# Kernel optimization log

Hardware: AMD Instinct MI355X
Metric: run time of the kernel (lower is better)

Reference implementation:

```python
import jax, jax.numpy as jnp
import numpy as np

N_HEADS = 16
HEAD_DIM = 64
ROPE_BASE = 10000.0
EPS = 1e-6


def _rope_tables(T, hd, dtype):
    inv_freq = 1.0 / (ROPE_BASE ** (jnp.arange(0, hd, 2, dtype=jnp.float32) / hd))
    freqs = jnp.arange(T, dtype=jnp.float32)[:, None] * inv_freq[None, :]  # [T, hd/2]
    cos = jnp.cos(freqs)[None, :, None, :].astype(dtype)  # [1,T,1,hd/2]
    sin = jnp.sin(freqs)[None, :, None, :].astype(dtype)
    return cos, sin


def _apply_rope(x, cos, sin):
    d = x.shape[-1] // 2
    x1, x2 = x[..., :d], x[..., d:]
    return jnp.concatenate([x1 * cos + x2 * sin, -x1 * sin + x2 * cos], axis=-1)


def setup_inputs() -> dict:
    key = jax.random.key(0)
    k1, k2, k3, k4 = jax.random.split(key, 4)
    B, T, C = 4, 1024, 1024
    x = jax.random.normal(k1, (B, T, C), dtype=jnp.float32)
    W_qkv = jax.random.normal(k2, (3 * C, C), dtype=jnp.float32) * (1.0 / np.sqrt(C))
    W_out = jax.random.normal(k3, (C, C), dtype=jnp.float32) * (1.0 / np.sqrt(C))
    # learnable per-head curvature, init = exp(randn) * base_curvature (base=1.0)
    hyp_k = jnp.exp(jax.random.normal(k4, (1, N_HEADS, 1, 1), dtype=jnp.float32))
    return {"x": x, "W_qkv": W_qkv, "W_out": W_out, "hyp_k": hyp_k}


def reference(x, W_qkv, W_out, hyp_k):
    B, T, C = x.shape
    H, hd = N_HEADS, HEAD_DIM
    qkv = x @ W_qkv.T  # [B,T,3C]
    q, k, v = jnp.split(qkv, 3, axis=-1)
    q = q.reshape(B, T, H, hd)
    k = k.reshape(B, T, H, hd)
    v = v.reshape(B, T, H, hd)

    cos, sin = _rope_tables(T, hd, x.dtype)
    q = _apply_rope(q, cos, sin)
    k = _apply_rope(k, cos, sin)

    # [B,H,T,hd]
    q = q.transpose(0, 2, 1, 3)
    k = k.transpose(0, 2, 1, 3)
    v = v.transpose(0, 2, 1, 3)

    # Lorentz lift: x0 = sqrt(k + ||x||^2); inner = -x0*y0 + <x,y>;
    # dist = sqrt(k) * arccosh(-inner / k)  (geoopt Lorentz convention)
    kc = hyp_k[:, :, :, 0]  # [1,H,1]
    q0 = jnp.sqrt(kc + jnp.sum(q * q, axis=-1))  # [B,H,T]
    k0 = jnp.sqrt(kc + jnp.sum(k * k, axis=-1))  # [B,H,T]
    inner = jnp.einsum('bhld,bhsd->bhls', q, k) - q0[..., None] * k0[:, :, None, :]
    arg = jnp.maximum(-inner / hyp_k, 1.0 + EPS)
    dis = jnp.sqrt(hyp_k) * jnp.arccosh(arg)  # [B,H,L,S]

    attn_weight = 1.0 / (EPS + dis)
    causal = jnp.tril(jnp.ones((T, T), dtype=bool))
    attn_weight = jnp.where(causal, attn_weight, -jnp.inf)
    attn = jax.nn.softmax(attn_weight, axis=-1)
    out = jnp.einsum('bhls,bhsd->bhld', attn, v)  # [B,H,T,hd]
    out = out.transpose(0, 2, 1, 3).reshape(B, T, C)
    return out @ W_out.T
```

## Files before the change

kernel.cpp:

```cpp
#include <hip/hip_runtime.h>

#define B_ 4
#define T_ 1024
#define C_ 1024
#define H_ 16
#define HD_ 64

typedef short bf16x8 __attribute__((ext_vector_type(8)));
typedef float f32x4 __attribute__((ext_vector_type(4)));

__device__ __forceinline__ ushort f2bf(float f) {
    union { float f; unsigned u; } v; v.f = f;
    unsigned u = v.u;
    unsigned r = (u + 0x7fffu + ((u >> 16) & 1u)) >> 16;
    return (ushort)r;
}

__device__ __forceinline__ f32x4 mfma16(bf16x8 a, bf16x8 b, f32x4 c) {
    return __builtin_amdgcn_mfma_f32_16x16x32_bf16(a, b, c, 0, 0, 0);
}

__device__ __forceinline__ bf16x8 lds_frag(const ushort* base, int row, int byteoff) {
    int addr = (row * 128 + byteoff) ^ ((row & 7) << 4);
    uint4 u = *(const uint4*)((const char*)base + addr);
    return __builtin_bit_cast(bf16x8, u);
}

__device__ __forceinline__ bf16x8 lds_frag_v(const ushort* base, int d, int byteoff) {
    int addr = (d * 128 + byteoff) ^ ((((d & 7) ^ (d >> 3)) & 7) << 4);
    uint4 u = *(const uint4*)((const char*)base + addr);
    return __builtin_bit_cast(bf16x8, u);
}

__device__ __forceinline__ bf16x8 lds_frag_p(const ushort* base, int row, int byteoff) {
    int addr = (row * 128 + byteoff) ^ (((row >> 2) & 3) << 5);
    uint4 u = *(const uint4*)((const char*)base + addr);
    return __builtin_bit_cast(bf16x8, u);
}

__device__ __forceinline__ void bar_plain() {
    __builtin_amdgcn_sched_barrier(0);
    __builtin_amdgcn_s_barrier();
    __builtin_amdgcn_sched_barrier(0);
}
__device__ __forceinline__ void bar_vm6() {
    asm volatile("s_waitcnt vmcnt(6)" ::: "memory");
    __builtin_amdgcn_sched_barrier(0);
    __builtin_amdgcn_s_barrier();
    __builtin_amdgcn_sched_barrier(0);
}
__device__ __forceinline__ void bar_vm0() {
    asm volatile("s_waitcnt vmcnt(0)" ::: "memory");
    __builtin_amdgcn_sched_barrier(0);
    __builtin_amdgcn_s_barrier();
    __builtin_amdgcn_sched_barrier(0);
}

__device__ __forceinline__ void stage128(ushort* sbase, const ushort* gtile, int wv, int lane) {
    const int srow = lane >> 3;
    const ushort* g0 = gtile + (size_t)srow * C_ + ((((lane & 7) ^ srow)) << 3);
#pragma unroll
    for (int i = 0; i < 4; ++i) {
        int w = wv * 4 + i;
        const ushort* g = g0 + (size_t)(w * 8) * C_;
        ushort* l = sbase + w * 512;
        __builtin_amdgcn_global_load_lds((const __attribute__((address_space(1))) void*)g,
                                         (__attribute__((address_space(3))) void*)l, 16, 0, 0);
    }
}
__device__ __forceinline__ void stage64(ushort* sbase, const ushort* gtile, int wv, int lane) {
    const int srow = lane >> 3;
    const ushort* g0 = gtile + (size_t)srow * C_ + ((((lane & 7) ^ srow)) << 3);
#pragma unroll
    for (int i = 0; i < 2; ++i) {
        int w = wv * 2 + i;
        const ushort* g = g0 + (size_t)(w * 8) * C_;
        ushort* l = sbase + w * 512;
        __builtin_amdgcn_global_load_lds((const __attribute__((address_space(1))) void*)g,
                                         (__attribute__((address_space(3))) void*)l, 16, 0, 0);
    }
}

__global__ void cast_all(const float* __restrict__ x, const float* __restrict__ wqkv,
                         const float* __restrict__ wout,
                         ushort* __restrict__ xb, ushort* __restrict__ wqkvb,
                         ushort* __restrict__ woutb) {
    int i = (blockIdx.x * 256 + threadIdx.x) * 4;
    const float* src; ushort* dst; int off;
    if (i < 4194304)      { src = x;    dst = xb;    off = i; }
    else if (i < 7340032) { src = wqkv; dst = wqkvb; off = i - 4194304; }
    else                  { src = wout; dst = woutb; off = i - 7340032; }
    float4 v = *(const float4*)(src + off);
    ushort4 o = make_ushort4(f2bf(v.x), f2bf(v.y), f2bf(v.z), f2bf(v.w));
    *(ushort4*)(dst + off) = o;
}

#define GEMM_COMPUTE_128x64(As, Bs)                                                       \
    {                                                                                     \
        _Pragma("unroll")                                                                 \
        for (int ks = 0; ks < 2; ++ks) {                                                  \
            bf16x8 af[2], bfr[4];                                                         \
            _Pragma("unroll")                                                             \
            for (int mf = 0; mf < 2; ++mf)                                                \
                af[mf] = lds_frag(As, wv * 32 + mf * 16 + (lane & 15),                    \
                                  ks * 64 + ((lane >> 4) << 4));                          \
            _Pragma("unroll")                                                             \
            for (int nf = 0; nf < 4; ++nf)                                                \
                bfr[nf] = lds_frag(Bs, nf * 16 + (lane & 15),                             \
                                   ks * 64 + ((lane >> 4) << 4));                         \
            _Pragma("unroll")                                                             \
            for (int mf = 0; mf < 2; ++mf)                                                \
                _Pragma("unroll")                                                         \
                for (int nf = 0; nf < 4; ++nf)                                            \
                    acc[mf][nf] = mfma16(af[mf], bfr[nf], acc[mf][nf]);                   \
        }                                                                                 \
    }

#define GEMM_DMA_LOOP()                                                                   \
    stage(As0, Bs0, 0);                                                                   \
    stage(As1, Bs1, 1);                                                                   \
    for (int kt = 0; kt < 14; kt += 2) {                                                  \
        bar_vm6();                                     \
        GEMM_COMPUTE_128x64(As0, Bs0);                                                    \
        bar_plain();                                     \
        stage(As0, Bs0, kt + 2);                                                          \
        bar_vm6();                                                     \
        GEMM_COMPUTE_128x64(As1, Bs1);                                                    \
        bar_plain();                                                                      \
        stage(As1, Bs1, kt + 3);                                          \
    }                                                                                     \
    bar_vm6();                                            \
    GEMM_COMPUTE_128x64(As0, Bs0);                                                        \
    bar_vm0();                                                            \
    GEMM_COMPUTE_128x64(As1, Bs1);

__global__ __launch_bounds__(256) void gemm_qkv(
    const ushort* __restrict__ Xb, const ushort* __restrict__ Wb,
    const float* __restrict__ hyp,
    ushort* __restrict__ Qo, ushort* __restrict__ Ko, ushort* __restrict__ Vo,
    float* __restrict__ q0g, float* __restrict__ k0g)
{
    __shared__ ushort As0[128 * 64], Bs0[64 * 64];
    __shared__ ushort As1[128 * 64], Bs1[64 * 64];
    const int tid = threadIdx.x, lane = tid & 63, wv = tid >> 6;
    const int m0 = blockIdx.x * 128, n0 = blockIdx.y * 64;
    const ushort* Asrc = Xb + (size_t)m0 * C_;
    const ushort* Bsrc = Wb + (size_t)n0 * C_;

    auto stage = [&](ushort* Ad, ushort* Bd, int kt) {
        stage128(Ad, Asrc + kt * 64, wv, lane);
        stage64(Bd, Bsrc + kt * 64, wv, lane);
    };

    f32x4 acc[2][4] = {};
    GEMM_DMA_LOOP();

    const int sector = n0 >> 10;
    const int h = (n0 & 1023) >> 6;
    const float kc = hyp[h];
    const float inv_k = 1.0f / kc;
    float invf[2];
    invf[0] = __expf(-0.28782313662425572f * (float)(lane & 15));
    invf[1] = __expf(-0.28782313662425572f * (float)(16 + (lane & 15)));

#pragma unroll
    for (int mf = 0; mf < 2; ++mf) {
        float o[4][4];
#pragma unroll
        for (int nf = 0; nf < 4; ++nf)
#pragma unroll
            for (int r = 0; r < 4; ++r) o[nf][r] = acc[mf][nf][r];

        if (sector < 2) {
#pragma unroll
            for (int p = 0; p < 2; ++p) {
#pragma unroll
                for (int r = 0; r < 4; ++r) {
                    int m = m0 + wv * 32 + mf * 16 + ((lane >> 4) << 2) + r;
                    int t = m & (T_ - 1);
                    float sn, cs; __sincosf((float)t * invf[p], &sn, &cs);
                    float x1 = o[p][r], x2 = o[p + 2][r];
                    o[p][r]     =  x1 * cs + x2 * sn;
                    o[p + 2][r] = -x1 * sn + x2 * cs;
                }
            }
        }

#pragma unroll
        for (int r = 0; r < 4; ++r) {
            int m = m0 + wv * 32 + mf * 16 + ((lane >> 4) << 2) + r;
            int b = m >> 10, t = m & (T_ - 1);
            int bh = b * H_ + h;
            size_t base = ((size_t)bh * T_ + t) * HD_;
            float nrm = 0.f;
#pragma unroll
            for (int nf = 0; nf < 4; ++nf) {
                int d = nf * 16 + (lane & 15);
                float v = o[nf][r];
                nrm += v * v;
                ushort bv = f2bf(sector == 1 ? v * inv_k : v);
                if (sector == 0)      Qo[base + d] = bv;
                else if (sector == 1) Ko[base + d] = bv;
                else                  Vo[base + d] = bv;
            }
            if (sector < 2) {
#pragma unroll
                for (int mk = 1; mk < 16; mk <<= 1) nrm += __shfl_xor(nrm, mk);
                if ((lane & 15) == 0) {
                    float v0 = sqrtf(kc + nrm);
                    if (sector == 0) q0g[(size_t)bh * T_ + t] = v0;
                    else             k0g[(size_t)bh * T_ + t] = v0 * inv_k;
                }
            }
        }
    }
}

__global__ __launch_bounds__(256) void gemm_out(
    const ushort* __restrict__ Ab, const ushort* __restrict__ Wb, float* __restrict__ Out)
{
    __shared__ ushort As0[128 * 64], Bs0[64 * 64];
    __shared__ ushort As1[128 * 64], Bs1[64 * 64];
    const int tid = threadIdx.x, lane = tid & 63, wv = tid >> 6;
    const int m0 = blockIdx.x * 128, n0 = blockIdx.y * 64;
    const ushort* Asrc = Ab + (size_t)m0 * C_;
    const ushort* Bsrc = Wb + (size_t)n0 * C_;

    auto stage = [&](ushort* Ad, ushort* Bd, int kt) {
        stage128(Ad, Asrc + kt * 64, wv, lane);
        stage64(Bd, Bsrc + kt * 64, wv, lane);
    };

    f32x4 acc[2][4] = {};
    GEMM_DMA_LOOP();

#pragma unroll
    for (int mf = 0; mf < 2; ++mf)
#pragma unroll
        for (int r = 0; r < 4; ++r) {
            int m = m0 + wv * 32 + mf * 16 + ((lane >> 4) << 2) + r;
#pragma unroll
            for (int nf = 0; nf < 4; ++nf) {
                int n = n0 + nf * 16 + (lane & 15);
                Out[(size_t)m * C_ + n] = acc[mf][nf][r];
            }
        }
}

__global__ __launch_bounds__(256, 2) void attn_fwd(
    const ushort* __restrict__ Q, const ushort* __restrict__ K, const ushort* __restrict__ V,
    const float* __restrict__ q0g, const float* __restrict__ k0g,
    const float* __restrict__ hyp, ushort* __restrict__ AO)
{
    __shared__ ushort Ks[64 * 64];
    __shared__ ushort Vts[64 * 64];
    __shared__ ushort Ps[4][16 * 64];
    __shared__ float k0s[64];

    const int tid = threadIdx.x, lane = tid & 63, wv = tid >> 6;
    const int pr = blockIdx.x >> 6;
    const int bh = blockIdx.x & 63;
    const int h = bh & (H_ - 1);
    const int qa = pr, qb = 15 - pr, nt = qb + 1;
    const float c3 = sqrtf(hyp[h]) * 0.48045301391820142f;
    const float e3 = 6.931471805599453e-07f;

    const ushort* Kb = K + (size_t)bh * T_ * HD_;
    const ushort* Vb = V + (size_t)bh * T_ * HD_;

    bf16x8 aqA[2], aqB[2];
    {
        const ushort* qA = Q + ((size_t)bh * T_ + qa * 64 + wv * 16 + (lane & 15)) * HD_;
        const ushort* qB = Q + ((size_t)bh * T_ + qb * 64 + wv * 16 + (lane & 15)) * HD_;
#pragma unroll
        for (int ks = 0; ks < 2; ++ks) {
            aqA[ks] = __builtin_bit_cast(bf16x8, *(const uint4*)(qA + ks * 32 + ((lane >> 4) << 3)));
            aqB[ks] = __builtin_bit_cast(bf16x8, *(const uint4*)(qB + ks * 32 + ((lane >> 4) << 3)));
        }
    }
    float q0A[4], q0B[4];
#pragma unroll
    for (int r = 0; r < 4; ++r) {
        int rr = wv * 16 + ((lane >> 4) << 2) + r;
        q0A[r] = q0g[(size_t)bh * T_ + qa * 64 + rr];
        q0B[r] = q0g[(size_t)bh * T_ + qb * 64 + rr];
    }

    f32x4 oaccA[4] = {}, oaccB[4] = {};
    float lpA[4] = {}, lpB[4] = {};

    const int krow = tid >> 3, koff = tid & 7;
    const int sp = tid >> 3, dc = tid & 7;
    uint4 kv0, kv1, vv0, vv1;
    float kz = 0.f;
    auto issue = [&](int s0) {
        kv0 = *(const uint4*)(Kb + (size_t)(s0 + krow) * HD_ + koff * 8);
        kv1 = *(const uint4*)(Kb + (size_t)(s0 + 32 + krow) * HD_ + koff * 8);
        vv0 = *(const uint4*)(Vb + (size_t)(s0 + 2 * sp) * HD_ + dc * 8);
        vv1 = *(const uint4*)(Vb + (size_t)(s0 + 2 * sp + 1) * HD_ + dc * 8);
        if (tid < 64) kz = k0g[(size_t)bh * T_ + s0 + tid];
    };

    auto geom = [&](const f32x4* sc, const float* q0, const float* k0r, float p[4][4]) {
#pragma unroll
        for (int r = 0; r < 4; ++r)
#pragma unroll
            for (int sf = 0; sf < 4; ++sf) {
                float arg = fmaf(q0[r], k0r[sf], -sc[sf][r]);
                arg = fmaxf(arg, 1.0f + 1e-6f);
                float t = fmaf(arg, arg, -1.0f);
                float u = arg + __builtin_amdgcn_sqrtf(t);
                float l2 = __builtin_amdgcn_logf(u);
                float w2 = fmaf(l2, c3, e3);
                float rv = fminf(__builtin_amdgcn_rcpf(w2), 30.0f);
                p[sf][r] = __builtin_amdgcn_exp2f(rv);
            }
    };
    auto mask_diag = [&](float p[4][4]) {
        const int qloc = wv * 16 + ((lane >> 4) << 2);
#pragma unroll
        for (int r = 0; r < 4; ++r)
#pragma unroll
            for (int sf = 0; sf < 4; ++sf)
                if (sf * 16 + (lane & 15) > qloc + r) p[sf][r] = 0.f;
    };
    auto pv_step = [&](float p[4][4], ushort* ps, const bf16x8 (&vf)[2][4],
                       f32x4* oacc, float* lp) {
#pragma unroll
        for (int r = 0; r < 4; ++r) {
            int row = ((lane >> 4) << 2) + r;
#pragma unroll
            for (int sf = 0; sf < 4; ++sf) {
                int addr = (row * 128 + (sf * 16 + (lane & 15)) * 2) ^ (((row >> 2) & 3) << 5);
                *(ushort*)((char*)ps + addr) = f2bf(p[sf][r]);
            }
            lp[r] += (p[0][r] + p[1][r]) + (p[2][r] + p[3][r]);
        }
#pragma unroll
        for (int ks = 0; ks < 2; ++ks) {
            bf16x8 ap = lds_frag_p(ps, lane & 15, ks * 64 + ((lane >> 4) << 4));
#pragma unroll
            for (int df = 0; df < 4; ++df)
                oacc[df] = mfma16(ap, vf[ks][df], oacc[df]);
        }
    };

    issue(0);

    for (int it = 0; it < nt; ++it) {
        const bool actA = (it <= qa);
        __syncthreads();
        {
            *(uint4*)((char*)Ks + ((tid * 16) ^ ((krow & 7) << 4))) = kv0;
            int c1 = tid + 256;
            *(uint4*)((char*)Ks + ((c1 * 16) ^ (((c1 >> 3) & 7) << 4))) = kv1;
            union { uint4 v; ushort u[8]; } a, b;
            a.v = vv0; b.v = vv1;
#pragma unroll
            for (int j = 0; j < 8; ++j) {
                int d = dc * 8 + j;
                uint pack = (uint)a.u[j] | ((uint)b.u[j] << 16);
                *(uint*)((char*)Vts + ((d * 128 + sp * 4) ^ (((j ^ dc) & 7) << 4))) = pack;
            }
            if (tid < 64) k0s[tid] = kz;
        }
        if (it + 1 < nt) issue((it + 1) * 64);
        __syncthreads();

        bf16x8 bk[2][4];
#pragma unroll
        for (int ks = 0; ks < 2; ++ks)
#pragma unroll
            for (int sf = 0; sf < 4; ++sf)
                bk[ks][sf] = lds_frag(Ks, sf * 16 + (lane & 15), ks * 64 + ((lane >> 4) << 4));

        float k0r[4];
#pragma unroll
        for (int sf = 0; sf < 4; ++sf) k0r[sf] = k0s[sf * 16 + (lane & 15)];

        f32x4 scB[4] = {};
#pragma unroll
        for (int ks = 0; ks < 2; ++ks)
#pragma unroll
            for (int sf = 0; sf < 4; ++sf)
                scB[sf] = mfma16(aqB[ks], bk[ks][sf], scB[sf]);
        f32x4 scA[4] = {};
        if (actA) {
#pragma unroll
            for (int ks = 0; ks < 2; ++ks)
#pragma unroll
                for (int sf = 0; sf < 4; ++sf)
                    scA[sf] = mfma16(aqA[ks], bk[ks][sf], scA[sf]);
        }

        bf16x8 vf[2][4];
#pragma unroll
        for (int ks = 0; ks < 2; ++ks)
#pragma unroll
            for (int df = 0; df < 4; ++df)
                vf[ks][df] = lds_frag_v(Vts, df * 16 + (lane & 15), ks * 64 + ((lane >> 4) << 4));

        float pB[4][4];
        geom(scB, q0B, k0r, pB);
        if (it == qb) mask_diag(pB);
        pv_step(pB, Ps[wv], vf, oaccB, lpB);

        if (actA) {
            float pA[4][4];
            geom(scA, q0A, k0r, pA);
            if (it == qa) mask_diag(pA);
            pv_step(pA, Ps[wv], vf, oaccA, lpA);
        }
    }

    const int b = bh >> 4;
    auto epi = [&](f32x4* oacc, float* lp, int qt) {
#pragma unroll
        for (int r = 0; r < 4; ++r) {
            float s = lp[r];
#pragma unroll
            for (int mk = 1; mk < 16; mk <<= 1) s += __shfl_xor(s, mk);
            float invl = __builtin_amdgcn_rcpf(s);
            int t = qt * 64 + wv * 16 + ((lane >> 4) << 2) + r;
            size_t base = ((size_t)b * T_ + t) * C_ + h * HD_;
#pragma unroll
            for (int df = 0; df < 4; ++df)
                AO[base + df * 16 + (lane & 15)] = f2bf(oacc[df][r] * invl);
        }
    };
    epi(oaccA, lpA, qa);
    epi(oaccB, lpB, qb);
}

extern "C" void kernel_launch(void* const* d_in, const int* in_sizes, int n_in,
                              void* d_out, int out_size, void* d_ws, size_t ws_size,
                              hipStream_t stream)
{
    const float* x    = (const float*)d_in[0];
    const float* wqkv = (const float*)d_in[1];
    const float* wout = (const float*)d_in[2];
    const float* hyp  = (const float*)d_in[3];

    char* ws = (char*)d_ws;
    ushort* xb    = (ushort*)(ws + 0);
    ushort* wqkvb = (ushort*)(ws + 8388608);
    ushort* woutb = (ushort*)(ws + 14680064);
    ushort* Qb    = (ushort*)(ws + 16777216);
    ushort* Kb    = (ushort*)(ws + 25165824);
    ushort* Vb    = (ushort*)(ws + 33554432);
    ushort* Ab    = (ushort*)(ws + 41943040);
    float*  q0    = (float*)(ws + 50331648);
    float*  k0    = (float*)(ws + 50593792);

    cast_all<<<8192, 256, 0, stream>>>(x, wqkv, wout, xb, wqkvb, woutb);

    gemm_qkv<<<dim3(32, 48), 256, 0, stream>>>(xb, wqkvb, hyp, Qb, Kb, Vb, q0, k0);
    attn_fwd<<<512, 256, 0, stream>>>(Qb, Kb, Vb, q0, k0, hyp, Ab);
    gemm_out<<<dim3(32, 16), 256, 0, stream>>>(Ab, woutb, (float*)d_out);
}
```

Before: 93.85 us.

## Split paired query tiles across two wave groups in 512-thread attention blocks

The attention kernel now launches 512 threads per block, and each group of four waves handles one of the two paired query tiles (qa or qb) instead of every wave processing both. K/V tiles are loaded once into shared memory and shared by both groups, with the K staging spread over all 512 threads. The intent is to halve per-wave serial work and register pressure while keeping K/V reuse. The cost is load imbalance: the qa group idles through most iterations but still joins the block barriers, and the launch bound of 2 blocks per CU is dropped.

```diff
diff --git a/kernel.cpp b/kernel.cpp
--- a/kernel.cpp
+++ b/kernel.cpp
@@ -120,18 +120,18 @@
     stage(As0, Bs0, 0);                                                                   \
     stage(As1, Bs1, 1);                                                                   \
     for (int kt = 0; kt < 14; kt += 2) {                                                  \
-        bar_vm6();                                     \
+        bar_vm6();                                                                        \
         GEMM_COMPUTE_128x64(As0, Bs0);                                                    \
-        bar_plain();                                     \
+        bar_plain();                                                                      \
         stage(As0, Bs0, kt + 2);                                                          \
-        bar_vm6();                                                     \
+        bar_vm6();                                                                        \
         GEMM_COMPUTE_128x64(As1, Bs1);                                                    \
         bar_plain();                                                                      \
-        stage(As1, Bs1, kt + 3);                                          \
+        stage(As1, Bs1, kt + 3);                                                          \
     }                                                                                     \
-    bar_vm6();                                            \
+    bar_vm6();                                                                            \
     GEMM_COMPUTE_128x64(As0, Bs0);                                                        \
-    bar_vm0();                                                            \
+    bar_vm0();                                                                            \
     GEMM_COMPUTE_128x64(As1, Bs1);
 
 __global__ __launch_bounds__(256) void gemm_qkv(
@@ -247,66 +247,64 @@
         }
 }
 
-__global__ __launch_bounds__(256, 2) void attn_fwd(
+__global__ __launch_bounds__(512) void attn_fwd(
     const ushort* __restrict__ Q, const ushort* __restrict__ K, const ushort* __restrict__ V,
     const float* __restrict__ q0g, const float* __restrict__ k0g,
     const float* __restrict__ hyp, ushort* __restrict__ AO)
 {
     __shared__ ushort Ks[64 * 64];
     __shared__ ushort Vts[64 * 64];
-    __shared__ ushort Ps[4][16 * 64];
+    __shared__ ushort Ps[8][16 * 64];
     __shared__ float k0s[64];
 
     const int tid = threadIdx.x, lane = tid & 63, wv = tid >> 6;
+    const int grp = wv >> 2, w4 = wv & 3;
     const int pr = blockIdx.x >> 6;
     const int bh = blockIdx.x & 63;
     const int h = bh & (H_ - 1);
     const int qa = pr, qb = 15 - pr, nt = qb + 1;
+    const int qt = grp ? qb : qa;
+    const int myNt = grp ? nt : (qa + 1);
     const float c3 = sqrtf(hyp[h]) * 0.48045301391820142f;
     const float e3 = 6.931471805599453e-07f;
 
     const ushort* Kb = K + (size_t)bh * T_ * HD_;
     const ushort* Vb = V + (size_t)bh * T_ * HD_;
 
-    bf16x8 aqA[2], aqB[2];
+    bf16x8 aq[2];
     {
-        const ushort* qA = Q + ((size_t)bh * T_ + qa * 64 + wv * 16 + (lane & 15)) * HD_;
-        const ushort* qB = Q + ((size_t)bh * T_ + qb * 64 + wv * 16 + (lane & 15)) * HD_;
-#pragma unroll
-        for (int ks = 0; ks < 2; ++ks) {
-            aqA[ks] = __builtin_bit_cast(bf16x8, *(const uint4*)(qA + ks * 32 + ((lane >> 4) << 3)));
-            aqB[ks] = __builtin_bit_cast(bf16x8, *(const uint4*)(qB + ks * 32 + ((lane >> 4) << 3)));
-        }
-    }
-    float q0A[4], q0B[4];
-#pragma unroll
-    for (int r = 0; r < 4; ++r) {
-        int rr = wv * 16 + ((lane >> 4) << 2) + r;
-        q0A[r] = q0g[(size_t)bh * T_ + qa * 64 + rr];
-        q0B[r] = q0g[(size_t)bh * T_ + qb * 64 + rr];
-    }
-
-    f32x4 oaccA[4] = {}, oaccB[4] = {};
-    float lpA[4] = {}, lpB[4] = {};
+        const ushort* qP = Q + ((size_t)bh * T_ + qt * 64 + w4 * 16 + (lane & 15)) * HD_;
+#pragma unroll
+        for (int ks = 0; ks < 2; ++ks)
+            aq[ks] = __builtin_bit_cast(bf16x8, *(const uint4*)(qP + ks * 32 + ((lane >> 4) << 3)));
+    }
+    float q0v[4];
+#pragma unroll
+    for (int r = 0; r < 4; ++r)
+        q0v[r] = q0g[(size_t)bh * T_ + qt * 64 + w4 * 16 + ((lane >> 4) << 2) + r];
+
+    f32x4 oacc[4] = {};
+    float lp[4] = {};
 
     const int krow = tid >> 3, koff = tid & 7;
     const int sp = tid >> 3, dc = tid & 7;
-    uint4 kv0, kv1, vv0, vv1;
+    uint4 kv, vv0, vv1;
     float kz = 0.f;
     auto issue = [&](int s0) {
-        kv0 = *(const uint4*)(Kb + (size_t)(s0 + krow) * HD_ + koff * 8);
-        kv1 = *(const uint4*)(Kb + (size_t)(s0 + 32 + krow) * HD_ + koff * 8);
-        vv0 = *(const uint4*)(Vb + (size_t)(s0 + 2 * sp) * HD_ + dc * 8);
-        vv1 = *(const uint4*)(Vb + (size_t)(s0 + 2 * sp + 1) * HD_ + dc * 8);
+        kv = *(const uint4*)(Kb + (size_t)(s0 + krow) * HD_ + koff * 8);
+        if (wv < 4) {
+            vv0 = *(const uint4*)(Vb + (size_t)(s0 + 2 * sp) * HD_ + dc * 8);
+            vv1 = *(const uint4*)(Vb + (size_t)(s0 + 2 * sp + 1) * HD_ + dc * 8);
+        }
         if (tid < 64) kz = k0g[(size_t)bh * T_ + s0 + tid];
     };
 
-    auto geom = [&](const f32x4* sc, const float* q0, const float* k0r, float p[4][4]) {
+    auto geom = [&](const f32x4* sc, const float* k0r, float p[4][4]) {
 #pragma unroll
         for (int r = 0; r < 4; ++r)
 #pragma unroll
             for (int sf = 0; sf < 4; ++sf) {
-                float arg = fmaf(q0[r], k0r[sf], -sc[sf][r]);
+                float arg = fmaf(q0v[r], k0r[sf], -sc[sf][r]);
                 arg = fmaxf(arg, 1.0f + 1e-6f);
                 float t = fmaf(arg, arg, -1.0f);
                 float u = arg + __builtin_amdgcn_sqrtf(t);
@@ -317,119 +315,99 @@
             }
     };
     auto mask_diag = [&](float p[4][4]) {
-        const int qloc = wv * 16 + ((lane >> 4) << 2);
+        const int qloc = w4 * 16 + ((lane >> 4) << 2);
 #pragma unroll
         for (int r = 0; r < 4; ++r)
 #pragma unroll
             for (int sf = 0; sf < 4; ++sf)
                 if (sf * 16 + (lane & 15) > qloc + r) p[sf][r] = 0.f;
     };
-    auto pv_step = [&](float p[4][4], ushort* ps, const bf16x8 (&vf)[2][4],
-                       f32x4* oacc, float* lp) {
-#pragma unroll
-        for (int r = 0; r < 4; ++r) {
-            int row = ((lane >> 4) << 2) + r;
-#pragma unroll
-            for (int sf = 0; sf < 4; ++sf) {
-                int addr = (row * 128 + (sf * 16 + (lane & 15)) * 2) ^ (((row >> 2) & 3) << 5);
-                *(ushort*)((char*)ps + addr) = f2bf(p[sf][r]);
-            }
-            lp[r] += (p[0][r] + p[1][r]) + (p[2][r] + p[3][r]);
-        }
-#pragma unroll
-        for (int ks = 0; ks < 2; ++ks) {
-            bf16x8 ap = lds_frag_p(ps, lane & 15, ks * 64 + ((lane >> 4) << 4));
-#pragma unroll
-            for (int df = 0; df < 4; ++df)
-                oacc[df] = mfma16(ap, vf[ks][df], oacc[df]);
-        }
-    };
 
     issue(0);
 
     for (int it = 0; it < nt; ++it) {
-        const bool actA = (it <= qa);
         __syncthreads();
         {
-            *(uint4*)((char*)Ks + ((tid * 16) ^ ((krow & 7) << 4))) = kv0;
-            int c1 = tid + 256;
-            *(uint4*)((char*)Ks + ((c1 * 16) ^ (((c1 >> 3) & 7) << 4))) = kv1;
-            union { uint4 v; ushort u[8]; } a, b;
-            a.v = vv0; b.v = vv1;
-#pragma unroll
-            for (int j = 0; j < 8; ++j) {
-                int d = dc * 8 + j;
-                uint pack = (uint)a.u[j] | ((uint)b.u[j] << 16);
-                *(uint*)((char*)Vts + ((d * 128 + sp * 4) ^ (((j ^ dc) & 7) << 4))) = pack;
+            *(uint4*)((char*)Ks + ((tid * 16) ^ ((krow & 7) << 4))) = kv;
+            if (wv < 4) {
+                union { uint4 v; ushort u[8]; } a, b;
+                a.v = vv0; b.v = vv1;
+#pragma unroll
+                for (int j = 0; j < 8; ++j) {
+                    int d = dc * 8 + j;
+                    uint pack = (uint)a.u[j] | ((uint)b.u[j] << 16);
+                    *(uint*)((char*)Vts + ((d * 128 + sp * 4) ^ (((j ^ dc) & 7) << 4))) = pack;
+                }
             }
             if (tid < 64) k0s[tid] = kz;
         }
         if (it + 1 < nt) issue((it + 1) * 64);
         __syncthreads();
 
-        bf16x8 bk[2][4];
-#pragma unroll
-        for (int ks = 0; ks < 2; ++ks)
-#pragma unroll
-            for (int sf = 0; sf < 4; ++sf)
-                bk[ks][sf] = lds_frag(Ks, sf * 16 + (lane & 15), ks * 64 + ((lane >> 4) << 4));
-
-        float k0r[4];
-#pragma unroll
-        for (int sf = 0; sf < 4; ++sf) k0r[sf] = k0s[sf * 16 + (lane & 15)];
-
-        f32x4 scB[4] = {};
-#pragma unroll
-        for (int ks = 0; ks < 2; ++ks)
-#pragma unroll
-            for (int sf = 0; sf < 4; ++sf)
-                scB[sf] = mfma16(aqB[ks], bk[ks][sf], scB[sf]);
-        f32x4 scA[4] = {};
-        if (actA) {
+        if (it < myNt) {
+            bf16x8 bk[2][4];
 #pragma unroll
             for (int ks = 0; ks < 2; ++ks)
 #pragma unroll
                 for (int sf = 0; sf < 4; ++sf)
-                    scA[sf] = mfma16(aqA[ks], bk[ks][sf], scA[sf]);
-        }
-
-        bf16x8 vf[2][4];
-#pragma unroll
-        for (int ks = 0; ks < 2; ++ks)
-#pragma unroll
-            for (int df = 0; df < 4; ++df)
-                vf[ks][df] = lds_frag_v(Vts, df * 16 + (lane & 15), ks * 64 + ((lane >> 4) << 4));
-
-        float pB[4][4];
-        geom(scB, q0B, k0r, pB);
-        if (it == qb) mask_diag(pB);
-        pv_step(pB, Ps[wv], vf, oaccB, lpB);
-
-        if (actA) {
-            float pA[4][4];
-            geom(scA, q0A, k0r, pA);
-            if (it == qa) mask_diag(pA);
-            pv_step(pA, Ps[wv], vf, oaccA, lpA);
+                    bk[ks][sf] = lds_frag(Ks, sf * 16 + (lane & 15), ks * 64 + ((lane >> 4) << 4));
+
+            float k0r[4];
+#pragma unroll
+            for (int sf = 0; sf < 4; ++sf) k0r[sf] = k0s[sf * 16 + (lane & 15)];
+
+            f32x4 sc[4] = {};
+#pragma unroll
+            for (int ks = 0; ks < 2; ++ks)
+#pragma unroll
+                for (int sf = 0; sf < 4; ++sf)
+                    sc[sf] = mfma16(aq[ks], bk[ks][sf], sc[sf]);
+
+            bf16x8 vf[2][4];
+#pragma unroll
+            for (int ks = 0; ks < 2; ++ks)
+#pragma unroll
+                for (int df = 0; df < 4; ++df)
+                    vf[ks][df] = lds_frag_v(Vts, df * 16 + (lane & 15), ks * 64 + ((lane >> 4) << 4));
+
+            float p[4][4];
+            geom(sc, k0r, p);
+            if (it == qt) mask_diag(p);
+
+            ushort* ps = Ps[wv];
+#pragma unroll
+            for (int r = 0; r < 4; ++r) {
+                int row = ((lane >> 4) << 2) + r;
+#pragma unroll
+                for (int sf = 0; sf < 4; ++sf) {
+                    int addr = (row * 128 + (sf * 16 + (lane & 15)) * 2) ^ (((row >> 2) & 3) << 5);
+                    *(ushort*)((char*)ps + addr) = f2bf(p[sf][r]);
+                }
+                lp[r] += (p[0][r] + p[1][r]) + (p[2][r] + p[3][r]);
+            }
+#pragma unroll
+            for (int ks = 0; ks < 2; ++ks) {
+                bf16x8 ap = lds_frag_p(ps, lane & 15, ks * 64 + ((lane >> 4) << 4));
+#pragma unroll
+                for (int df = 0; df < 4; ++df)
+                    oacc[df] = mfma16(ap, vf[ks][df], oacc[df]);
+            }
         }
     }
 
     const int b = bh >> 4;
-    auto epi = [&](f32x4* oacc, float* lp, int qt) {
-#pragma unroll
-        for (int r = 0; r < 4; ++r) {
-            float s = lp[r];
-#pragma unroll
-            for (int mk = 1; mk < 16; mk <<= 1) s += __shfl_xor(s, mk);
-            float invl = __builtin_amdgcn_rcpf(s);
-            int t = qt * 64 + wv * 16 + ((lane >> 4) << 2) + r;
-            size_t base = ((size_t)b * T_ + t) * C_ + h * HD_;
-#pragma unroll
-            for (int df = 0; df < 4; ++df)
-                AO[base + df * 16 + (lane & 15)] = f2bf(oacc[df][r] * invl);
-        }
-    };
-    epi(oaccA, lpA, qa);
-    epi(oaccB, lpB, qb);
+#pragma unroll
+    for (int r = 0; r < 4; ++r) {
+        float s = lp[r];
+#pragma unroll
+        for (int mk = 1; mk < 16; mk <<= 1) s += __shfl_xor(s, mk);
+        float invl = __builtin_amdgcn_rcpf(s);
+        int t = qt * 64 + w4 * 16 + ((lane >> 4) << 2) + r;
+        size_t base = ((size_t)b * T_ + t) * C_ + h * HD_;
+#pragma unroll
+        for (int df = 0; df < 4; ++df)
+            AO[base + df * 16 + (lane & 15)] = f2bf(oacc[df][r] * invl);
+    }
 }
 
 extern "C" void kernel_launch(void* const* d_in, const int* in_sizes, int n_in,
@@ -455,6 +433,6 @@
     cast_all<<<8192, 256, 0, stream>>>(x, wqkv, wout, xb, wqkvb, woutb);
 
     gemm_qkv<<<dim3(32, 48), 256, 0, stream>>>(xb, wqkvb, hyp, Qb, Kb, Vb, q0, k0);
-    attn_fwd<<<512, 256, 0, stream>>>(Qb, Kb, Vb, q0, k0, hyp, Ab);
+    attn_fwd<<<512, 512, 0, stream>>>(Qb, Kb, Vb, q0, k0, hyp, Ab);
     gemm_out<<<dim3(32, 16), 256, 0, stream>>>(Ab, woutb, (float*)d_out);
 }
```

Measured after the change: 98.58 us. 1.05x slower.
